# Optimization experiments

Hardware: AMD Instinct MI355X
Metric: run time of the kernel (lower is better)

The kernel has to match this reference:

```python
import jax, jax.numpy as jnp
import numpy as np

SC = 11  # window stride / block size; unfold kernel = 3*SC = 33, padding = SC


def _unfold3(x, sc):
    """Equivalent of nn.Unfold(kernel=3*sc, stride=sc, padding=sc) on [b,c,H,W]
    where H, W are multiples of sc. Returns [b, c, 9*sc*sc, n_windows].
    Patch ordering within K differs from torch by a fixed permutation, which is
    immaterial: all contractions over K (mask, softmax, value aggregation) are
    permutation-invariant as long as the same unfold is used everywhere."""
    b, c, H, W = x.shape
    h_sc, w_sc = H // sc, W // sc
    xp = jnp.pad(x, ((0, 0), (0, 0), (sc, sc), (sc, sc)))
    blk = xp.reshape(b, c, h_sc + 2, sc, w_sc + 2, sc)
    # 3x3 neighborhood of sc-blocks around each window
    pat = jnp.stack([blk[:, :, di:di + h_sc, :, dj:dj + w_sc, :]
                     for di in range(3) for dj in range(3)], axis=2)
    # [b,c,9,h_sc,r,w_sc,s] -> [b,c,9,r,s,h_sc,w_sc] -> [b,c,9*sc*sc,n]
    pat = pat.transpose(0, 1, 2, 4, 6, 3, 5)
    return pat.reshape(b, c, 9 * sc * sc, h_sc * w_sc)


def _block_q(x, sc):
    """view(b,c,h_sc,sc,w_sc,sc).permute(0,1,2,4,3,5) -> [b,c,n,sc*sc]"""
    b, c, H, W = x.shape
    h_sc, w_sc = H // sc, W // sc
    y = x.reshape(b, c, h_sc, sc, w_sc, sc).transpose(0, 1, 2, 4, 3, 5)
    return y.reshape(b, c, h_sc * w_sc, sc * sc)


def setup_inputs() -> dict:
    key = jax.random.key(0)
    k1, k2, k3, k4, k5, k6 = jax.random.split(key, 6)
    b, c, h, w = 2, 64, 256, 256
    s = 1.0 / np.sqrt(c)
    return {
        "x_key": jax.random.normal(k1, (b, c, h, w), jnp.float32),
        "x_ref": jax.random.normal(k2, (b, c, h, w), jnp.float32),
        "Wq": jax.random.normal(k3, (c, c), jnp.float32) * s,
        "Wk": jax.random.normal(k4, (c, c), jnp.float32) * s,
        "Wv": jax.random.normal(k5, (c, c), jnp.float32) * s,
        "gamma": jax.random.normal(k6, (1,), jnp.float32) * 0.1,
    }


def reference(x_key, x_ref, Wq, Wk, Wv, gamma):
    sc = SC
    b, c, h_in, w_in = x_key.shape
    x_pad = sc - w_in % sc
    y_pad = sc - h_in % sc
    pad = ((0, 0), (0, 0), (0, y_pad), (0, x_pad))
    fk = jnp.pad(x_key, pad)
    fr = jnp.pad(x_ref, pad)
    b, c, h, w = fk.shape
    h_sc, w_sc = h // sc, w // sc

    # validity mask -> additive attention bias (out-of-image keys penalized)
    fm = jnp.pad(jnp.ones((1, 1, h_in, w_in), fk.dtype), pad)
    fm_k = _unfold3(fm, sc)          # [1,1,K,n]
    fm_q = _block_q(fm, sc)          # [1,1,n,s]
    am = (jnp.einsum('bckn,bcns->bkns', fm_k, fm_q) - 1.0) * 99.0  # [1,K,n,s]

    scale = c ** (-0.5)
    q = jnp.einsum('oi,bihw->bohw', Wq, fk)
    k = jnp.einsum('oi,bihw->bohw', Wk, fr)
    v = jnp.einsum('oi,bihw->bohw', Wv, fr)

    k_u = _unfold3(k, sc) * scale    # [b,c,K,n]
    q_b = _block_q(q, sc)            # [b,c,n,s]
    attn = jnp.einsum('bckn,bcns->bkns', k_u, q_b) + am  # [b,K,n,s]
    attn = jax.nn.softmax(attn, axis=1)

    v_u = _unfold3(v, sc)            # [b,c,K,n]
    r = jnp.einsum('bkns,bckn->bcns', attn, v_u)  # [b,c,n,s]
    r = r.reshape(b, c, h_sc, w_sc, sc, sc).transpose(0, 1, 2, 4, 3, 5)
    r = r.reshape(b, c, h, w)[:, :, :h_in, :w_in]
    return x_ref + r * gamma[0]
```

## Files before the change

### kernel.cpp

```cpp
#include <hip/hip_runtime.h>


typedef unsigned short ushort_t;
typedef unsigned int   uint32;
typedef __attribute__((ext_vector_type(8))) short short8;
typedef __attribute__((ext_vector_type(4))) float f32x4;

#define MFMA16(a,b,c) __builtin_amdgcn_mfma_f32_16x16x32_bf16(a,b,c,0,0,0)

#if __has_builtin(__builtin_amdgcn_exp2f)
#define EXP2(x) __builtin_amdgcn_exp2f(x)
#else
#define EXP2(x) exp2f(x)
#endif
#if __has_builtin(__builtin_amdgcn_rcpf)
#define RCP(x) __builtin_amdgcn_rcpf(x)
#else
#define RCP(x) (1.0f/(x))
#endif

#define QPKT_OFF   0u
#define KPKT_OFF   18874368u
#define VPKT_OFF   37748736u

__device__ __forceinline__ ushort_t f2bf(float f){
  uint32 u = __float_as_uint(f);
  u = (u + 0x7FFFu + ((u >> 16) & 1u)) >> 16;
  return (ushort_t)u;
}

__device__ __forceinline__ uint32 pkbf(float a, float b){
#if __has_builtin(__builtin_amdgcn_cvt_pk_bf16_f32)
  typedef __attribute__((ext_vector_type(2))) __bf16 bf2;
  union { bf2 v; uint32 u; } c;
  c.v = __builtin_amdgcn_cvt_pk_bf16_f32(a, b);
  return c.u;
#else
  return (uint32)f2bf(a) | ((uint32)f2bf(b) << 16);
#endif
}

__device__ __forceinline__ void storeK8(ushort_t* __restrict__ base, int nt, int t,
                                        int l15, int h, f32x4 a){
  uint32 lo = pkbf(a[0], a[1]);
  uint32 hi = pkbf(a[2], a[3]);
  int lanep = l15 + 16*((2*t + (h>>1)) & 3);
  size_t off = (size_t)((nt*2 + (t>>1))*64 + lanep)*16 + 8*(h&1);
  *(uint2*)((char*)base + off) = make_uint2(lo, hi);
}

__device__ __forceinline__ short8 ldWfrag(const float* __restrict__ W, int t, int ks,
                                          int l15, int h, float scale){
  const float* p = W + (16*t + l15)*64 + 32*ks + 8*h;
  float4 a = *(const float4*)p;
  float4 b = *(const float4*)(p + 4);
  union { uint4 u; short8 s; } x;
  x.u.x = pkbf(a.x*scale, a.y*scale);
  x.u.y = pkbf(a.z*scale, a.w*scale);
  x.u.z = pkbf(b.x*scale, b.y*scale);
  x.u.w = pkbf(b.z*scale, b.w*scale);
  return x.s;
}

__global__ __launch_bounds__(256) void proj_kernel(
    const float* __restrict__ xk, const float* __restrict__ xr,
    const float* __restrict__ Wq, const float* __restrict__ Wk, const float* __restrict__ Wv,
    ushort_t* __restrict__ qpkt, ushort_t* __restrict__ kpkt, ushort_t* __restrict__ vpkt)
{
  __shared__ __align__(16) float sX[64*192];
  const int tid = threadIdx.x;
  const int lane = tid & 63, wv = tid >> 6;
  const int l15 = lane & 15, h = lane >> 4;
  const int bid = blockIdx.x;
  const bool isQ = bid >= 1152;
  const int id = isQ ? bid - 1152 : bid;
  const int b = id / 576, rem = id % 576, ty = rem / 24, tx = rem % 24;
  const float* xs = (isQ ? xk : xr) + (size_t)b*64*65536;
  const int oy = ty*11, ox = tx*11;
  const int ox3 = ox & 3, xa = ox - ox3;

  #pragma unroll
  for (int i = tid; i < 1024; i += 256) sX[(i>>4)*192 + 176 + (i&15)] = 0.f;

  {
    const int ch = tid >> 2, seg = tid & 3;
    const float* rowp = xs + (size_t)ch*65536 + (size_t)oy*256 + (xa + 4*seg);
    float* sdst = sX + ch*192 + 4*seg;
    if (ty < 23 && tx < 23){
      #pragma unroll
      for (int y = 0; y < 11; ++y)
        *(float4*)(sdst + y*16) = *(const float4*)(rowp + y*256);
    } else {
      const int xg = xa + 4*seg;
      #pragma unroll
      for (int y = 0; y < 11; ++y){
        const bool rk = (oy + y) < 256;
        float4 v;
        v.x = (rk && xg+0 < 256) ? rowp[y*256+0] : 0.f;
        v.y = (rk && xg+1 < 256) ? rowp[y*256+1] : 0.f;
        v.z = (rk && xg+2 < 256) ? rowp[y*256+2] : 0.f;
        v.w = (rk && xg+3 < 256) ? rowp[y*256+3] : 0.f;
        *(float4*)(sdst + y*16) = v;
      }
    }
  }
  __syncthreads();

  const f32x4 zero = {0.f, 0.f, 0.f, 0.f};
  #define XFL(nt, ks, dst) { \
    const int px_ = 16*(nt) + l15; \
    const int y_ = (px_*745) >> 13; \
    const float* pp_ = sX + (32*(ks) + 8*h)*192 + y_*16 + (px_ - y_*11) + ox3; \
    union { uint4 u; short8 s; } r_; \
    r_.u.x = pkbf(pp_[0],    pp_[192]); \
    r_.u.y = pkbf(pp_[384],  pp_[576]); \
    r_.u.z = pkbf(pp_[768],  pp_[960]); \
    r_.u.w = pkbf(pp_[1152], pp_[1344]); \
    dst = r_.s; }

  if (!isQ){
    short8 wkf[4][2], wvf[4][2];
    #pragma unroll
    for (int t = 0; t < 4; ++t){
      wkf[t][0] = ldWfrag(Wk, t, 0, l15, h, 1.f);  wkf[t][1] = ldWfrag(Wk, t, 1, l15, h, 1.f);
      wvf[t][0] = ldWfrag(Wv, t, 0, l15, h, 1.f);  wvf[t][1] = ldWfrag(Wv, t, 1, l15, h, 1.f);
    }
    ushort_t* kb = kpkt + (size_t)id*8192;
    ushort_t* vb = vpkt + (size_t)id*8192;
    const int nt0 = 2*wv, nt1 = 2*wv + 1;
    short8 xf0[2], xf1[2];
    XFL(nt0, 0, xf0[0]); XFL(nt0, 1, xf0[1]);
    XFL(nt1, 0, xf1[0]); XFL(nt1, 1, xf1[1]);
    #pragma unroll
    for (int t = 0; t < 4; ++t){
      f32x4 ak0 = MFMA16(wkf[t][0], xf0[0], zero); ak0 = MFMA16(wkf[t][1], xf0[1], ak0);
      f32x4 ak1 = MFMA16(wkf[t][0], xf1[0], zero); ak1 = MFMA16(wkf[t][1], xf1[1], ak1);
      f32x4 av0 = MFMA16(xf0[0], wvf[t][0], zero); av0 = MFMA16(xf0[1], wvf[t][1], av0);
      f32x4 av1 = MFMA16(xf1[0], wvf[t][0], zero); av1 = MFMA16(xf1[1], wvf[t][1], av1);
      storeK8(kb, nt0, t, l15, h, ak0);
      storeK8(kb, nt1, t, l15, h, ak1);
      uint4 pv;
      pv.x = pkbf(av0[0], av0[1]); pv.y = pkbf(av0[2], av0[3]);
      pv.z = pkbf(av1[0], av1[1]); pv.w = pkbf(av1[2], av1[3]);
      *(uint4*)((char*)vb + (size_t)((wv*4 + t)*64 + lane)*16) = pv;
    }
  } else {
    const float C1 = 0.18033688011112042f;
    short8 wqf[4][2];
    #pragma unroll
    for (int t = 0; t < 4; ++t){
      wqf[t][0] = ldWfrag(Wq, t, 0, l15, h, C1);  wqf[t][1] = ldWfrag(Wq, t, 1, l15, h, C1);
    }
    ushort_t* qb = qpkt + (size_t)id*8192;
    #pragma unroll
    for (int nn = 0; nn < 2; ++nn){
      const int nt = 2*wv + nn;
      short8 xf[2];
      XFL(nt, 0, xf[0]); XFL(nt, 1, xf[1]);
      #pragma unroll
      for (int t = 0; t < 4; ++t){
        f32x4 aq = MFMA16(wqf[t][0], xf[0], zero); aq = MFMA16(wqf[t][1], xf[1], aq);
        storeK8(qb, nt, t, l15, h, aq);
      }
    }
  }
  #undef XFL
}

__global__ __launch_bounds__(64) void attn_kernel(
    ushort_t* qpkt,
    const ushort_t* __restrict__ kpkt, const ushort_t* __restrict__ vpkt,
    const float* __restrict__ gamma)
{
  const int lane = threadIdx.x;
  const int g = (blockIdx.x & 7)*288 + (blockIdx.x >> 3);
  const int win = g >> 1, wave = g & 1;
  const int b = win / 576, wid = win % 576, wy = wid / 24, wx = wid % 24;
  const int l15 = lane & 15, h = lane >> 4;

  short8 qf[4][2];
  {
    const ushort_t* qblk = qpkt + (size_t)win*8192;
    #pragma unroll
    for (int mt = 0; mt < 4; ++mt){
      qf[mt][0] = *(const short8*)(qblk + (size_t)(((4*wave+mt)*2 + 0)*64 + lane)*8);
      qf[mt][1] = *(const short8*)(qblk + (size_t)(((4*wave+mt)*2 + 1)*64 + lane)*8);
    }
  }

  f32x4 o[4][4];
  float lsum[4] = {0.f, 0.f, 0.f, 0.f};
  #pragma unroll
  for (int mt = 0; mt < 4; ++mt)
    #pragma unroll
    for (int u = 0; u < 4; ++u) o[mt][u] = (f32x4){0.f,0.f,0.f,0.f};

  const f32x4 zz = {0.f,0.f,0.f,0.f};

  #pragma unroll 1
  for (int ck = 0; ck < 9; ++ck){
    const int ty = wy - 1 + ck/3, tx = wx - 1 + ck%3;
    if ((unsigned)ty >= 24u || (unsigned)tx >= 24u) continue;
    const size_t tbase = (size_t)(b*576 + ty*24 + tx)*8192;
    const char* kg = (const char*)(kpkt + tbase);
    const char* vg = (const char*)(vpkt + tbase);
    const bool ey = (ty == 23), ex = (tx == 23);

    #pragma unroll
    for (int ntp = 0; ntp < 4; ++ntp){
      short8 kf00 = *(const short8*)(kg + ((4*ntp+0)*64 + lane)*16);
      short8 kf01 = *(const short8*)(kg + ((4*ntp+1)*64 + lane)*16);
      short8 kf10 = *(const short8*)(kg + ((4*ntp+2)*64 + lane)*16);
      short8 kf11 = *(const short8*)(kg + ((4*ntp+3)*64 + lane)*16);
      short8 vf0  = *(const short8*)(vg + ((4*ntp+0)*64 + lane)*16);
      short8 vf1  = *(const short8*)(vg + ((4*ntp+1)*64 + lane)*16);
      short8 vf2  = *(const short8*)(vg + ((4*ntp+2)*64 + lane)*16);
      short8 vf3  = *(const short8*)(vg + ((4*ntp+3)*64 + lane)*16);

      bool okk[8];
      #pragma unroll
      for (int kt = 0; kt < 2; ++kt)
        #pragma unroll
        for (int r = 0; r < 4; ++r){
          const int kl = 32*ntp + 16*kt + 4*h + r;
          bool ok = kl < 121;
          if (ey | ex){
            const int ky = (kl*745) >> 13, kx = kl - ky*11;
            if (ey) ok = ok && (ky < 3);
            if (ex) ok = ok && (kx < 3);
          }
          okk[4*kt + r] = ok;
        }

      #pragma unroll
      for (int mt = 0; mt < 4; ++mt){
        f32x4 s0 = MFMA16(kf00, qf[mt][0], zz); s0 = MFMA16(kf01, qf[mt][1], s0);
        f32x4 s1 = MFMA16(kf10, qf[mt][0], zz); s1 = MFMA16(kf11, qf[mt][1], s1);
        float p[8];
        #pragma unroll
        for (int r = 0; r < 4; ++r){
          p[r]   = okk[r]   ? EXP2(s0[r]) : 0.f;
          p[4+r] = okk[4+r] ? EXP2(s1[r]) : 0.f;
        }
        lsum[mt] += ((p[0]+p[1]) + (p[2]+p[3])) + ((p[4]+p[5]) + (p[6]+p[7]));
        union { uint4 u; short8 s; } af;
        af.u.x = pkbf(p[0], p[1]); af.u.y = pkbf(p[2], p[3]);
        af.u.z = pkbf(p[4], p[5]); af.u.w = pkbf(p[6], p[7]);
        o[mt][0] = MFMA16(af.s, vf0, o[mt][0]);
        o[mt][1] = MFMA16(af.s, vf1, o[mt][1]);
        o[mt][2] = MFMA16(af.s, vf2, o[mt][2]);
        o[mt][3] = MFMA16(af.s, vf3, o[mt][3]);
      }
    }
  }

  const float gm = gamma[0];
  ushort_t* rb = qpkt + (size_t)win*8192 + (size_t)wave*4096;
  #pragma unroll
  for (int mt = 0; mt < 4; ++mt){
    float v = lsum[mt];
    v += __shfl_xor(v, 16); v += __shfl_xor(v, 32);
    #pragma unroll
    for (int r = 0; r < 4; ++r){
      const float den = __shfl(v, 4*h + r);
      const float wg = gm * RCP(den);
      const int qs = 16*mt + 4*h + r;
      #pragma unroll
      for (int u = 0; u < 4; ++u)
        rb[(size_t)qs*64 + 16*u + l15] = f2bf(wg * o[mt][u][r]);
    }
  }
}

__global__ __launch_bounds__(256) void ep_kernel(
    const float* __restrict__ xref, const ushort_t* __restrict__ rbuf,
    float* __restrict__ out)
{
  __shared__ float tile[64][65];
  const int tid = threadIdx.x;
  const int bidx = blockIdx.x;
  const int xc = bidx & 3, y = (bidx >> 2) & 255, b = bidx >> 10;
  const int wy = (y*745) >> 13, qy = y - wy*11;
  {
    const int ch = tid & 63, xs4 = tid >> 6;
    #pragma unroll
    for (int xi = 0; xi < 16; ++xi){
      const int xl = xi*4 + xs4;
      const int x = xc*64 + xl;
      const int wx = (x*745) >> 13, qx = x - wx*11;
      const size_t ridx = (size_t)(b*576 + wy*24 + wx)*8192 + (size_t)(qy*11 + qx)*64 + ch;
      tile[xl][ch] = __uint_as_float(((uint32)rbuf[ridx]) << 16);
    }
  }
  __syncthreads();
  {
    const int xl = tid & 63, cg = tid >> 6;
    const size_t base = (size_t)b*4194304 + (size_t)y*256 + xc*64 + xl;
    #pragma unroll
    for (int ci = 0; ci < 16; ++ci){
      const int c2 = ci*4 + cg;
      const size_t idx = base + (size_t)c2*65536;
      out[idx] = xref[idx] + tile[xl][c2];
    }
  }
}

extern "C" void kernel_launch(void* const* d_in, const int* in_sizes, int n_in,
                              void* d_out, int out_size, void* d_ws, size_t ws_size,
                              hipStream_t stream)
{
  const float* xk = (const float*)d_in[0];
  const float* xr = (const float*)d_in[1];
  const float* Wq = (const float*)d_in[2];
  const float* Wk = (const float*)d_in[3];
  const float* Wv = (const float*)d_in[4];
  const float* gm = (const float*)d_in[5];
  float* out = (float*)d_out;
  char* ws = (char*)d_ws;
  ushort_t* qp = (ushort_t*)(ws + QPKT_OFF);
  ushort_t* kp = (ushort_t*)(ws + KPKT_OFF);
  ushort_t* vp = (ushort_t*)(ws + VPKT_OFF);
  (void)in_sizes; (void)n_in; (void)out_size; (void)ws_size;

  proj_kernel<<<2304, 256, 0, stream>>>(xk, xr, Wq, Wk, Wv, qp, kp, vp);
  attn_kernel<<<2304, 64, 0, stream>>>(qp, kp, vp, gm);
  ep_kernel<<<2048, 256, 0, stream>>>(xr, qp, out);
}
```

Baseline: 261.9 us.

## Share K/V tiles between window waves via double-buffered async LDS staging

Merges the two waves serving one window into a single 128-thread block. K and V neighbor tiles are loaded once into shared memory with direct global-to-LDS async loads: one wave stages K and the other stages V, double-buffered in half-tiles so the next load overlaps compute. Before this, each wave read K and V from global memory on its own. The change halves redundant global/L2 traffic and hides load latency, but adds barriers and LDS usage that may lower occupancy.

```diff
diff --git a/kernel.cpp b/kernel.cpp
--- a/kernel.cpp
+++ b/kernel.cpp
@@ -3,6 +3,7 @@
 
 typedef unsigned short ushort_t;
 typedef unsigned int   uint32;
+typedef unsigned long long uint64;
 typedef __attribute__((ext_vector_type(8))) short short8;
 typedef __attribute__((ext_vector_type(4))) float f32x4;
 
@@ -167,14 +168,15 @@
   #undef XFL
 }
 
-__global__ __launch_bounds__(64) void attn_kernel(
+__global__ __launch_bounds__(128) void attn_kernel(
     ushort_t* qpkt,
     const ushort_t* __restrict__ kpkt, const ushort_t* __restrict__ vpkt,
     const float* __restrict__ gamma)
 {
-  const int lane = threadIdx.x;
-  const int g = (blockIdx.x & 7)*288 + (blockIdx.x >> 3);
-  const int win = g >> 1, wave = g & 1;
+  __shared__ __align__(16) char smem[32768];
+  const int tid = threadIdx.x;
+  const int lane = tid & 63, wave = tid >> 6;
+  const int win = (blockIdx.x & 7)*144 + (blockIdx.x >> 3);
   const int b = win / 576, wid = win % 576, wy = wid / 24, wx = wid % 24;
   const int l15 = lane & 15, h = lane >> 4;
 
@@ -187,6 +189,16 @@
       qf[mt][1] = *(const short8*)(qblk + (size_t)(((4*wave+mt)*2 + 1)*64 + lane)*8);
     }
   }
+
+  uint64 cks = 0; int nv = 0;
+  #pragma unroll
+  for (int ck = 0; ck < 9; ++ck){
+    const int ty = wy - 1 + ck/3, tx = wx - 1 + ck%3;
+    if ((unsigned)ty < 24u && (unsigned)tx < 24u){
+      cks |= ((uint64)ck) << (4*nv); ++nv;
+    }
+  }
+  const int nu = 2*nv;
 
   f32x4 o[4][4];
   float lsum[4] = {0.f, 0.f, 0.f, 0.f};
@@ -194,28 +206,56 @@
   for (int mt = 0; mt < 4; ++mt)
     #pragma unroll
     for (int u = 0; u < 4; ++u) o[mt][u] = (f32x4){0.f,0.f,0.f,0.f};
-
   const f32x4 zz = {0.f,0.f,0.f,0.f};
 
+  const ushort_t* gsrcbase = wave ? vpkt : kpkt;
+  const int ldsw = wave ? 8192 : 0;
+
+  #define STAGE(u, bu) { \
+    const int t_ = (u) >> 1, hf_ = (u) & 1; \
+    const int ck_ = (int)((cks >> (4*t_)) & 15); \
+    const int cy_ = (ck_*11) >> 5; \
+    const int ty_ = wy - 1 + cy_, tx_ = wx - 1 + (ck_ - 3*cy_); \
+    const char* g_ = (const char*)(gsrcbase + (size_t)(b*576 + ty_*24 + tx_)*8192) \
+                     + hf_*8192 + lane*16; \
+    char* l_ = smem + (bu)*16384 + ldsw; \
+    _Pragma("unroll") \
+    for (int i_ = 0; i_ < 8; ++i_) \
+      __builtin_amdgcn_global_load_lds( \
+        (const __attribute__((address_space(1))) uint32*)(g_ + i_*1024), \
+        (__attribute__((address_space(3))) uint32*)(l_ + i_*1024), 16, 0, 0); \
+  }
+
+  STAGE(0, 0);
+  STAGE(1, 1);
+
   #pragma unroll 1
-  for (int ck = 0; ck < 9; ++ck){
-    const int ty = wy - 1 + ck/3, tx = wx - 1 + ck%3;
-    if ((unsigned)ty >= 24u || (unsigned)tx >= 24u) continue;
-    const size_t tbase = (size_t)(b*576 + ty*24 + tx)*8192;
-    const char* kg = (const char*)(kpkt + tbase);
-    const char* vg = (const char*)(vpkt + tbase);
-    const bool ey = (ty == 23), ex = (tx == 23);
-
-    #pragma unroll
-    for (int ntp = 0; ntp < 4; ++ntp){
-      short8 kf00 = *(const short8*)(kg + ((4*ntp+0)*64 + lane)*16);
-      short8 kf01 = *(const short8*)(kg + ((4*ntp+1)*64 + lane)*16);
-      short8 kf10 = *(const short8*)(kg + ((4*ntp+2)*64 + lane)*16);
-      short8 kf11 = *(const short8*)(kg + ((4*ntp+3)*64 + lane)*16);
-      short8 vf0  = *(const short8*)(vg + ((4*ntp+0)*64 + lane)*16);
-      short8 vf1  = *(const short8*)(vg + ((4*ntp+1)*64 + lane)*16);
-      short8 vf2  = *(const short8*)(vg + ((4*ntp+2)*64 + lane)*16);
-      short8 vf3  = *(const short8*)(vg + ((4*ntp+3)*64 + lane)*16);
+  for (int u = 0; u < nu; ++u){
+    const int bu = u & 1;
+    if (u + 1 < nu) { __asm__ volatile("s_waitcnt vmcnt(8)" ::: "memory"); }
+    else            { __asm__ volatile("s_waitcnt vmcnt(0)" ::: "memory"); }
+    __builtin_amdgcn_s_barrier();
+    __asm__ volatile("" ::: "memory");
+
+    const int t = u >> 1, hf = u & 1;
+    const int ckv = (int)((cks >> (4*t)) & 15);
+    const int cyv = (ckv*11) >> 5;
+    const int tyv = wy - 1 + cyv, txv = wx - 1 + (ckv - 3*cyv);
+    const bool ey = (tyv == 23), ex = (txv == 23);
+    const char* lk = smem + bu*16384;
+    const char* lv = lk + 8192;
+
+    #pragma unroll
+    for (int ntpl = 0; ntpl < 2; ++ntpl){
+      const int ntp = 2*hf + ntpl;
+      short8 kf00 = *(const short8*)(lk + ((4*ntpl+0)*64 + lane)*16);
+      short8 kf01 = *(const short8*)(lk + ((4*ntpl+1)*64 + lane)*16);
+      short8 kf10 = *(const short8*)(lk + ((4*ntpl+2)*64 + lane)*16);
+      short8 kf11 = *(const short8*)(lk + ((4*ntpl+3)*64 + lane)*16);
+      short8 vf0  = *(const short8*)(lv + ((4*ntpl+0)*64 + lane)*16);
+      short8 vf1  = *(const short8*)(lv + ((4*ntpl+1)*64 + lane)*16);
+      short8 vf2  = *(const short8*)(lv + ((4*ntpl+2)*64 + lane)*16);
+      short8 vf3  = *(const short8*)(lv + ((4*ntpl+3)*64 + lane)*16);
 
       bool okk[8];
       #pragma unroll
@@ -243,16 +283,21 @@
           p[4+r] = okk[4+r] ? EXP2(s1[r]) : 0.f;
         }
         lsum[mt] += ((p[0]+p[1]) + (p[2]+p[3])) + ((p[4]+p[5]) + (p[6]+p[7]));
-        union { uint4 u; short8 s; } af;
-        af.u.x = pkbf(p[0], p[1]); af.u.y = pkbf(p[2], p[3]);
-        af.u.z = pkbf(p[4], p[5]); af.u.w = pkbf(p[6], p[7]);
+        union { uint4 uu; short8 s; } af;
+        af.uu.x = pkbf(p[0], p[1]); af.uu.y = pkbf(p[2], p[3]);
+        af.uu.z = pkbf(p[4], p[5]); af.uu.w = pkbf(p[6], p[7]);
         o[mt][0] = MFMA16(af.s, vf0, o[mt][0]);
         o[mt][1] = MFMA16(af.s, vf1, o[mt][1]);
         o[mt][2] = MFMA16(af.s, vf2, o[mt][2]);
         o[mt][3] = MFMA16(af.s, vf3, o[mt][3]);
       }
     }
-  }
+
+    __asm__ volatile("" ::: "memory");
+    __builtin_amdgcn_s_barrier();
+    if (u + 2 < nu) STAGE(u + 2, bu);
+  }
+  #undef STAGE
 
   const float gm = gamma[0];
   ushort_t* rb = qpkt + (size_t)win*8192 + (size_t)wave*4096;
@@ -323,6 +368,6 @@
   (void)in_sizes; (void)n_in; (void)out_size; (void)ws_size;
 
   proj_kernel<<<2304, 256, 0, stream>>>(xk, xr, Wq, Wk, Wv, qp, kp, vp);
-  attn_kernel<<<2304, 64, 0, stream>>>(qp, kp, vp, gm);
+  attn_kernel<<<1152, 128, 0, stream>>>(qp, kp, vp, gm);
   ep_kernel<<<2048, 256, 0, stream>>>(xr, qp, out);
 }
```

Measured after the change: 251.1 us. 1.04x faster.
